# Optimization experiments

Measured on AMD Instinct MI355X. Metric: run time of the kernel, lower is better.

The kernel has to match this reference:

```python
import jax, jax.numpy as jnp
import numpy as np

N_NODES = 100000
N_EDGES = 1600000
IN_DIM, HID_DIM, OUT_DIM = 64, 128, 1


def gcn_conv(x, W, b, src, dst, n_nodes):
    """PyG-style GCNConv: h = x @ W; out = D^-1/2 (A+I) D^-1/2 h + b.
    Self-loops handled analytically (message h_i * dinv_i^2) to avoid
    concatenating them onto the edge list."""
    h = x @ W  # [N, F_out]
    ones = jnp.ones((src.shape[0],), dtype=x.dtype)
    deg = jax.ops.segment_sum(ones, dst, num_segments=n_nodes) + 1.0  # +1 self-loop
    dinv = jax.lax.rsqrt(deg)  # deg >= 1 so always finite
    norm = dinv[src] * dinv[dst]  # [E]
    msgs = h[src] * norm[:, None]  # [E, F_out] gather + scale
    agg = jax.ops.segment_sum(msgs, dst, num_segments=n_nodes)  # scatter-add
    agg = agg + h * (dinv * dinv)[:, None]  # self-loop contribution
    return agg + b


def setup_inputs() -> dict:
    key = jax.random.key(0)
    k1, k2, k3, k4 = jax.random.split(key, 4)
    x = jax.random.normal(k1, (N_NODES, IN_DIM), dtype=jnp.float32)
    edge_index = jax.random.randint(k2, (2, N_EDGES), 0, N_NODES, dtype=jnp.int64)
    # Glorot-ish init for weights
    W1 = jax.random.normal(k3, (IN_DIM, HID_DIM), dtype=jnp.float32) / np.sqrt(IN_DIM)
    b1 = jnp.zeros((HID_DIM,), dtype=jnp.float32)
    W2 = jax.random.normal(k4, (HID_DIM, OUT_DIM), dtype=jnp.float32) / np.sqrt(HID_DIM)
    b2 = jnp.zeros((OUT_DIM,), dtype=jnp.float32)
    return {"x": x, "edge_index": edge_index, "W1": W1, "b1": b1, "W2": W2, "b2": b2}


def reference(x, edge_index, W1, b1, W2, b2):
    src, dst = edge_index[0], edge_index[1]
    h = gcn_conv(x, W1, b1, src, dst, N_NODES)
    h = jax.nn.relu(h)
    # dropout(0.3) in eval mode == identity
    out = gcn_conv(h, W2, b2, src, dst, N_NODES)
    return out.reshape(-1)  # [N]
```

## Files before the change

### kernel.cpp

```cpp
#include <hip/hip_runtime.h>
#include <hip/hip_bf16.h>

#define NNODES 100000
#define NEDGES 1600000
#define IN_DIM 64
#define HID_DIM 128

#define BUKSHIFT 8
#define BUKNODES 256
#define NBUK ((NNODES + 255) >> 8)
#define BUKCAP 4608
#define CHUNK 4096
#define TILE_N 128
#define W1TS 72

#define EPACK(s, d)  ((s) | (((d) & 255) << 24))
#define ESRC(p)      ((p) & 0x00FFFFFF)
#define EDL(p)       ((int)(((unsigned)(p)) >> 24))

typedef __attribute__((ext_vector_type(8))) short short8;
typedef __attribute__((ext_vector_type(4))) float f32x4;

__device__ inline unsigned short f2bf(float f) {
    unsigned u = __float_as_uint(f);
    u += 0x7fff + ((u >> 16) & 1);
    return (unsigned short)(u >> 16);
}
__device__ inline unsigned bfpack2(float a, float b) {
    return (unsigned)f2bf(a) | ((unsigned)f2bf(b) << 16);
}
__device__ inline float bflo(unsigned u) { return __uint_as_float(u << 16); }
__device__ inline float bfhi(unsigned u) { return __uint_as_float(u & 0xffff0000u); }
__device__ inline float bfu16(unsigned v) { return __uint_as_float(v << 16); }

__global__ __launch_bounds__(1024, 8) void k_part(const int* __restrict__ src,
                                                  const int* __restrict__ dst,
                                                  int* __restrict__ gbcur,
                                                  int* __restrict__ ebuf, int E) {
    __shared__ int stage[CHUNK];
    __shared__ unsigned short bukof[CHUNK];
    __shared__ int hist[NBUK];
    __shared__ int scanb[NBUK];
    __shared__ int basep[NBUK];
    __shared__ int sb[2][512];
    int t = threadIdx.x;
    int start = blockIdx.x * CHUNK;
    int n = E - start; if (n > CHUNK) n = CHUNK;

    if (t < NBUK) hist[t] = 0;
    __syncthreads();

    int myb[4], myr[4], mp[4];
    #pragma unroll
    for (int i = 0; i < 4; i++) {
        int c = t + i * 1024;
        if (c < n) {
            int s = src[start + c];
            int d = dst[start + c];
            int b = d >> BUKSHIFT;
            myb[i] = b;
            mp[i]  = EPACK(s, d);
            myr[i] = atomicAdd(&hist[b], 1);
        } else myb[i] = -1;
    }
    __syncthreads();

    {
        int v = (t < NBUK) ? hist[t] : 0;
        if (t < 512) sb[0][t] = v;
        __syncthreads();
        int pin = 0;
        for (int ofs = 1; ofs < 512; ofs <<= 1) {
            if (t < 512) sb[pin ^ 1][t] = (t >= ofs) ? sb[pin][t] + sb[pin][t - ofs]
                                                     : sb[pin][t];
            __syncthreads();
            pin ^= 1;
        }
        if (t < NBUK) scanb[t] = sb[pin][t] - v;
    }

    if (t < NBUK) {
        int h = hist[t];
        basep[t] = h ? (t * BUKCAP + atomicAdd(&gbcur[t], h)) : 0;
    }
    __syncthreads();

    #pragma unroll
    for (int i = 0; i < 4; i++) {
        if (myb[i] >= 0) {
            int p = scanb[myb[i]] + myr[i];
            stage[p] = mp[i];
            bukof[p] = (unsigned short)myb[i];
        }
    }
    __syncthreads();

    for (int c = t; c < n; c += 1024) {
        int b = bukof[c];
        ebuf[basep[b] + (c - scanb[b])] = stage[c];
    }
}

__global__ __launch_bounds__(1024, 8) void k_bfill(const int* __restrict__ gbcur,
                                                   const int* __restrict__ ebuf,
                                                   const float* __restrict__ x,
                                                   int* __restrict__ off,
                                                   int* __restrict__ nend,
                                                   float* __restrict__ dinv,
                                                   int* __restrict__ csr,
                                                   unsigned* __restrict__ xsb, int N) {
    __shared__ int sEdge[BUKCAP];
    __shared__ int lcnt[BUKNODES];
    __shared__ int sbuf[2][BUKNODES];
    __shared__ int cur[BUKNODES];
    __shared__ float sdinv[BUKNODES];
    int b = blockIdx.x, t = threadIdx.x;
    int nbase = b << BUKSHIFT;
    int rbase = b * BUKCAP;
    int cntb = gbcur[b];
    if (t < BUKNODES) lcnt[t] = 0;
    __syncthreads();
    for (int i = t; i < cntb; i += 1024) {
        int p = ebuf[rbase + i];
        sEdge[i] = p;
        atomicAdd(&lcnt[EDL(p)], 1);
    }
    __syncthreads();
    int v = (t < BUKNODES) ? lcnt[t] : 0;
    if (t < BUKNODES) sbuf[0][t] = v;
    __syncthreads();
    int pin = 0;
    for (int ofs = 1; ofs < BUKNODES; ofs <<= 1) {
        if (t < BUKNODES) sbuf[pin ^ 1][t] = (t >= ofs) ? sbuf[pin][t] + sbuf[pin][t - ofs]
                                                        : sbuf[pin][t];
        __syncthreads();
        pin ^= 1;
    }
    if (t < BUKNODES) {
        int o = rbase + sbuf[pin][t] - v;
        int nid = nbase + t;
        float dv = rsqrtf((float)v + 1.0f);
        sdinv[t] = dv;
        if (nid < N) {
            off[nid]  = o;
            nend[nid] = o + v;
            dinv[nid] = dv;
        }
        cur[t] = o;
    }
    __syncthreads();
    for (int i = t; i < cntb; i += 1024) {
        int p = sEdge[i];
        int pos = atomicAdd(&cur[EDL(p)], 1);
        csr[pos] = ESRC(p);
    }
    for (int i = t; i < BUKNODES * 16; i += 1024) {
        int nl = i >> 4;
        int nid = nbase + nl;
        if (nid < N) {
            float dv = sdinv[nl];
            float4 vx = ((const float4*)x)[(size_t)nid * 16 + (i & 15)];
            uint2 u;
            u.x = bfpack2(vx.x * dv, vx.y * dv);
            u.y = bfpack2(vx.z * dv, vx.w * dv);
            ((uint2*)xsb)[(size_t)nid * 16 + (i & 15)] = u;
        }
    }
}

__global__ __launch_bounds__(256) void k_gathd(const int* __restrict__ off,
                                               const int* __restrict__ nend,
                                               const int* __restrict__ csr,
                                               const unsigned short* __restrict__ xsu,
                                               const float* __restrict__ dinv,
                                               unsigned short* __restrict__ aggu,
                                               int n_nodes) {
    int tid = blockIdx.x * 256 + threadIdx.x;
    int n = tid >> 6;
    if (n >= n_nodes) return;
    int lane = threadIdx.x & 63;
    int beg = off[n], fin = nend[n];
    float dd = dinv[n];

    float a0 = bfu16(xsu[(size_t)n * 64 + lane]);
    float a1 = 0.f, a2 = 0.f, a3 = 0.f;

    for (int base = beg; base < fin; base += 64) {
        int nn = fin - base; if (nn > 64) nn = 64;
        int idx = (lane < nn) ? csr[base + lane] : 0;
        int j = 0;
        for (; j + 4 <= nn; j += 4) {
            int s0 = __shfl(idx, j);
            int s1 = __shfl(idx, j + 1);
            int s2 = __shfl(idx, j + 2);
            int s3 = __shfl(idx, j + 3);
            unsigned v0 = xsu[(size_t)s0 * 64 + lane];
            unsigned v1 = xsu[(size_t)s1 * 64 + lane];
            unsigned v2 = xsu[(size_t)s2 * 64 + lane];
            unsigned v3 = xsu[(size_t)s3 * 64 + lane];
            a0 += bfu16(v0);
            a1 += bfu16(v1);
            a2 += bfu16(v2);
            a3 += bfu16(v3);
        }
        for (; j < nn; ++j) {
            int s = __shfl(idx, j);
            a0 += bfu16(xsu[(size_t)s * 64 + lane]);
        }
    }
    float r = ((a0 + a1) + (a2 + a3)) * dd;
    aggu[(size_t)n * 64 + lane] = f2bf(r);
}

__global__ __launch_bounds__(512) void k_mlp(const uint4* __restrict__ aggb,
                                             const float* __restrict__ W1,
                                             const float* __restrict__ b1,
                                             const float* __restrict__ W2,
                                             const float* __restrict__ dinv,
                                             float* __restrict__ zd, int n_nodes) {
    __shared__ __align__(16) unsigned short sW1t[HID_DIM * W1TS];
    __shared__ float sW2[HID_DIM];
    __shared__ float sb1[HID_DIM];
    int t = threadIdx.x;
    for (int i = t; i < IN_DIM * HID_DIM; i += 512) {
        int k = i >> 7, hid = i & 127;
        sW1t[hid * W1TS + k] = f2bf(W1[i]);
    }
    if (t < HID_DIM) { sW2[t] = W2[t]; sb1[t] = b1[t]; }
    __syncthreads();

    int node0 = blockIdx.x * TILE_N;
    int w = t >> 6;
    int lane = t & 63;
    int col = lane & 15;
    int quad = lane >> 4;

    int na = node0 + w * 16 + col;
    int nac = na < n_nodes ? na : 0;
    const short8* arow = (const short8*)(aggb + (size_t)nac * 8);
    short8 a0 = arow[quad];
    short8 a1 = arow[4 + quad];

    float zpart[4] = {0, 0, 0, 0};
    #pragma unroll
    for (int h0 = 0; h0 < 8; h0++) {
        int hid = h0 * 16 + col;
        const short8* brow = (const short8*)(sW1t + hid * W1TS);
        short8 b0 = brow[quad];
        short8 b1f = brow[4 + quad];
        f32x4 cc = {0.f, 0.f, 0.f, 0.f};
        cc = __builtin_amdgcn_mfma_f32_16x16x32_bf16(a0, b0, cc, 0, 0, 0);
        cc = __builtin_amdgcn_mfma_f32_16x16x32_bf16(a1, b1f, cc, 0, 0, 0);
        float bb = sb1[hid], ww = sW2[hid];
        #pragma unroll
        for (int r = 0; r < 4; r++) {
            float v = cc[r] + bb;
            zpart[r] += (v > 0.f ? v : 0.f) * ww;
        }
    }
    #pragma unroll
    for (int m = 1; m < 16; m <<= 1) {
        #pragma unroll
        for (int r = 0; r < 4; r++) zpart[r] += __shfl_xor(zpart[r], m);
    }
    if (col == 0) {
        #pragma unroll
        for (int r = 0; r < 4; r++) {
            int n = node0 + w * 16 + quad * 4 + r;
            if (n < n_nodes) zd[n] = zpart[r] * dinv[n];
        }
    }
}

__global__ __launch_bounds__(1024, 8) void k_gather1(const int* __restrict__ off,
                                                     const int* __restrict__ nend,
                                                     const int* __restrict__ csr,
                                                     const float* __restrict__ zd,
                                                     const float* __restrict__ dinv,
                                                     const float* __restrict__ b2,
                                                     float* __restrict__ out, int n_nodes) {
    int tid = blockIdx.x * 1024 + threadIdx.x;
    int n = tid >> 3;
    int l = tid & 7;
    if (n >= n_nodes) return;
    int beg = off[n], fin = nend[n];
    float a0 = 0.0f, a1 = 0.0f;
    for (int i = beg + l; i < fin; i += 16) {
        a0 += zd[csr[i]];
        int i2 = i + 8;
        if (i2 < fin) a1 += zd[csr[i2]];
    }
    float a = a0 + a1;
    a += __shfl_xor(a, 1);
    a += __shfl_xor(a, 2);
    a += __shfl_xor(a, 4);
    if (l == 0) out[n] = (a + zd[n]) * dinv[n] + b2[0];
}

extern "C" void kernel_launch(void* const* d_in, const int* in_sizes, int n_in,
                              void* d_out, int out_size, void* d_ws, size_t ws_size,
                              hipStream_t stream) {
    const float* x  = (const float*)d_in[0];
    const int*   ei = (const int*)d_in[1];
    const float* W1 = (const float*)d_in[2];
    const float* b1 = (const float*)d_in[3];
    const float* W2 = (const float*)d_in[4];
    const float* b2 = (const float*)d_in[5];
    float* out = (float*)d_out;

    const int N = NNODES;
    const int E = NEDGES;
    const int* src = ei;
    const int* dst = ei + E;

    int* gbcur = (int*)d_ws;
    int* off   = gbcur + 512;
    int* nend  = off + N;
    float* dinv = (float*)(nend + N);
    float* zd   = dinv + N;
    int* csr    = (int*)(zd + N);
    size_t o1 = ((size_t)((char*)(csr + NBUK * BUKCAP) - (char*)d_ws) + 127) & ~(size_t)127;
    unsigned* xsb = (unsigned*)((char*)d_ws + o1);
    size_t o2 = o1 + (size_t)N * 128;
    int*   ebuf = (int*)((char*)d_ws + o2);
    unsigned short* aggu = (unsigned short*)((char*)d_ws + o2);

    hipMemsetAsync(gbcur, 0, 512 * sizeof(int), stream);
    k_part<<<(E + CHUNK - 1) / CHUNK, 1024, 0, stream>>>(src, dst, gbcur, ebuf, E);
    k_bfill<<<NBUK, 1024, 0, stream>>>(gbcur, ebuf, x, off, nend, dinv, csr, xsb, N);
    k_gathd<<<(N * 64 + 255) / 256, 256, 0, stream>>>(off, nend, csr,
                                                      (const unsigned short*)xsb, dinv,
                                                      aggu, N);
    k_mlp<<<(N + TILE_N - 1) / TILE_N, 512, 0, stream>>>((const uint4*)aggu, W1, b1, W2,
                                                         dinv, zd, N);
    k_gather1<<<(N * 8 + 1023) / 1024, 1024, 0, stream>>>(off, nend, csr, zd, dinv, b2, out, N);
}
```

Before: 177.9 us.

## Replace CSR gather with bucketed LDS integer-atomic aggregation on int16-quantized features

The first-layer aggregation no longer does a per-node CSR gather. It now runs one block per 128-node bucket, reading the bucketed edge buffer directly and accumulating neighbour features into shared memory with integer atomics. The pre-scaled features are stored as fixed-point int16 (scale 4096, clamped) instead of bf16, which makes the integer LDS atomics exact and order-independent. Bucket size is halved to keep the accumulator in LDS, and the partition scan is widened to match. The risks are LDS atomic contention, precision loss and clamping for large scaled inputs, and a bucket capacity of 2432 that may overflow for skewed degree distributions.

```diff
diff --git a/kernel.cpp b/kernel.cpp
--- a/kernel.cpp
+++ b/kernel.cpp
@@ -6,15 +6,17 @@
 #define IN_DIM 64
 #define HID_DIM 128
 
-#define BUKSHIFT 8
-#define BUKNODES 256
-#define NBUK ((NNODES + 255) >> 8)
-#define BUKCAP 4608
+#define BUKSHIFT 7
+#define BUKNODES 128
+#define NBUK ((NNODES + 127) >> 7)
+#define BUKCAP 2432
 #define CHUNK 4096
 #define TILE_N 128
 #define W1TS 72
-
-#define EPACK(s, d)  ((s) | (((d) & 255) << 24))
+#define ACCS 66
+#define QS 4096.0f
+
+#define EPACK(s, d)  ((s) | (((d) & 127) << 24))
 #define ESRC(p)      ((p) & 0x00FFFFFF)
 #define EDL(p)       ((int)(((unsigned)(p)) >> 24))
 
@@ -29,9 +31,10 @@
 __device__ inline unsigned bfpack2(float a, float b) {
     return (unsigned)f2bf(a) | ((unsigned)f2bf(b) << 16);
 }
-__device__ inline float bflo(unsigned u) { return __uint_as_float(u << 16); }
-__device__ inline float bfhi(unsigned u) { return __uint_as_float(u & 0xffff0000u); }
-__device__ inline float bfu16(unsigned v) { return __uint_as_float(v << 16); }
+__device__ inline int f2i12(float v) {
+    float c = fminf(fmaxf(v * QS, -32767.f), 32767.f);
+    return __float2int_rn(c);
+}
 
 __global__ __launch_bounds__(1024, 8) void k_part(const int* __restrict__ src,
                                                   const int* __restrict__ dst,
@@ -42,7 +45,7 @@
     __shared__ int hist[NBUK];
     __shared__ int scanb[NBUK];
     __shared__ int basep[NBUK];
-    __shared__ int sb[2][512];
+    __shared__ int sb[2][1024];
     int t = threadIdx.x;
     int start = blockIdx.x * CHUNK;
     int n = E - start; if (n > CHUNK) n = CHUNK;
@@ -67,12 +70,11 @@
 
     {
         int v = (t < NBUK) ? hist[t] : 0;
-        if (t < 512) sb[0][t] = v;
+        sb[0][t] = v;
         __syncthreads();
         int pin = 0;
-        for (int ofs = 1; ofs < 512; ofs <<= 1) {
-            if (t < 512) sb[pin ^ 1][t] = (t >= ofs) ? sb[pin][t] + sb[pin][t - ofs]
-                                                     : sb[pin][t];
+        for (int ofs = 1; ofs < 1024; ofs <<= 1) {
+            sb[pin ^ 1][t] = (t >= ofs) ? sb[pin][t] + sb[pin][t - ofs] : sb[pin][t];
             __syncthreads();
             pin ^= 1;
         }
@@ -108,7 +110,7 @@
                                                    int* __restrict__ nend,
                                                    float* __restrict__ dinv,
                                                    int* __restrict__ csr,
-                                                   unsigned* __restrict__ xsb, int N) {
+                                                   short* __restrict__ xsq, int N) {
     __shared__ int sEdge[BUKCAP];
     __shared__ int lcnt[BUKNODES];
     __shared__ int sbuf[2][BUKNODES];
@@ -160,56 +162,77 @@
         if (nid < N) {
             float dv = sdinv[nl];
             float4 vx = ((const float4*)x)[(size_t)nid * 16 + (i & 15)];
+            int q0 = f2i12(vx.x * dv), q1 = f2i12(vx.y * dv);
+            int q2 = f2i12(vx.z * dv), q3 = f2i12(vx.w * dv);
             uint2 u;
-            u.x = bfpack2(vx.x * dv, vx.y * dv);
-            u.y = bfpack2(vx.z * dv, vx.w * dv);
-            ((uint2*)xsb)[(size_t)nid * 16 + (i & 15)] = u;
-        }
-    }
-}
-
-__global__ __launch_bounds__(256) void k_gathd(const int* __restrict__ off,
-                                               const int* __restrict__ nend,
-                                               const int* __restrict__ csr,
-                                               const unsigned short* __restrict__ xsu,
-                                               const float* __restrict__ dinv,
-                                               unsigned short* __restrict__ aggu,
-                                               int n_nodes) {
-    int tid = blockIdx.x * 256 + threadIdx.x;
-    int n = tid >> 6;
-    if (n >= n_nodes) return;
-    int lane = threadIdx.x & 63;
-    int beg = off[n], fin = nend[n];
-    float dd = dinv[n];
-
-    float a0 = bfu16(xsu[(size_t)n * 64 + lane]);
-    float a1 = 0.f, a2 = 0.f, a3 = 0.f;
-
-    for (int base = beg; base < fin; base += 64) {
-        int nn = fin - base; if (nn > 64) nn = 64;
-        int idx = (lane < nn) ? csr[base + lane] : 0;
-        int j = 0;
-        for (; j + 4 <= nn; j += 4) {
-            int s0 = __shfl(idx, j);
-            int s1 = __shfl(idx, j + 1);
-            int s2 = __shfl(idx, j + 2);
-            int s3 = __shfl(idx, j + 3);
-            unsigned v0 = xsu[(size_t)s0 * 64 + lane];
-            unsigned v1 = xsu[(size_t)s1 * 64 + lane];
-            unsigned v2 = xsu[(size_t)s2 * 64 + lane];
-            unsigned v3 = xsu[(size_t)s3 * 64 + lane];
-            a0 += bfu16(v0);
-            a1 += bfu16(v1);
-            a2 += bfu16(v2);
-            a3 += bfu16(v3);
-        }
-        for (; j < nn; ++j) {
-            int s = __shfl(idx, j);
-            a0 += bfu16(xsu[(size_t)s * 64 + lane]);
-        }
-    }
-    float r = ((a0 + a1) + (a2 + a3)) * dd;
-    aggu[(size_t)n * 64 + lane] = f2bf(r);
+            u.x = (q0 & 0xffff) | (q1 << 16);
+            u.y = (q2 & 0xffff) | (q3 << 16);
+            ((uint2*)xsq)[(size_t)nid * 16 + (i & 15)] = u;
+        }
+    }
+}
+
+__global__ __launch_bounds__(512, 8) void k_agg(const int* __restrict__ gbcur,
+                                                const int* __restrict__ ebuf,
+                                                const short* __restrict__ xsq,
+                                                const float* __restrict__ dinv,
+                                                unsigned short* __restrict__ aggu, int N) {
+    __shared__ int acc[BUKNODES * ACCS];
+    int b = blockIdx.x, t = threadIdx.x;
+    int rbase = b * BUKCAP;
+    int cntb = gbcur[b];
+    for (int i = t; i < BUKNODES * ACCS; i += 512) acc[i] = 0;
+    __syncthreads();
+
+    int c = t & 7;
+    int g = t >> 3;
+    const uint4* xq4 = (const uint4*)xsq;
+    for (int base = 0; base < cntb; base += 128) {
+        int e0 = base + g, e1 = base + 64 + g;
+        bool v0 = e0 < cntb, v1 = e1 < cntb;
+        int p0 = v0 ? ebuf[rbase + e0] : 0;
+        int p1 = v1 ? ebuf[rbase + e1] : 0;
+        uint4 ua = {0, 0, 0, 0}, ub = {0, 0, 0, 0};
+        if (v0) ua = xq4[(size_t)ESRC(p0) * 8 + c];
+        if (v1) ub = xq4[(size_t)ESRC(p1) * 8 + c];
+        if (v0) {
+            int* ar = &acc[EDL(p0) * ACCS + c * 8];
+            atomicAdd(&ar[0], (int)(short)(ua.x & 0xffff));
+            atomicAdd(&ar[1], ((int)ua.x) >> 16);
+            atomicAdd(&ar[2], (int)(short)(ua.y & 0xffff));
+            atomicAdd(&ar[3], ((int)ua.y) >> 16);
+            atomicAdd(&ar[4], (int)(short)(ua.z & 0xffff));
+            atomicAdd(&ar[5], ((int)ua.z) >> 16);
+            atomicAdd(&ar[6], (int)(short)(ua.w & 0xffff));
+            atomicAdd(&ar[7], ((int)ua.w) >> 16);
+        }
+        if (v1) {
+            int* ar = &acc[EDL(p1) * ACCS + c * 8];
+            atomicAdd(&ar[0], (int)(short)(ub.x & 0xffff));
+            atomicAdd(&ar[1], ((int)ub.x) >> 16);
+            atomicAdd(&ar[2], (int)(short)(ub.y & 0xffff));
+            atomicAdd(&ar[3], ((int)ub.y) >> 16);
+            atomicAdd(&ar[4], (int)(short)(ub.z & 0xffff));
+            atomicAdd(&ar[5], ((int)ub.z) >> 16);
+            atomicAdd(&ar[6], (int)(short)(ub.w & 0xffff));
+            atomicAdd(&ar[7], ((int)ub.w) >> 16);
+        }
+    }
+    __syncthreads();
+
+    int nbase = b << BUKSHIFT;
+    for (int i = t; i < BUKNODES * 32; i += 512) {
+        int dl = i >> 5, dp = i & 31;
+        int n = nbase + dl;
+        if (n < N) {
+            float dd = dinv[n] * (1.0f / QS);
+            int sp = ((const int*)xsq)[(size_t)n * 32 + dp];
+            int s0 = (sp << 16) >> 16, s1 = sp >> 16;
+            int A0 = acc[dl * ACCS + 2 * dp], A1 = acc[dl * ACCS + 2 * dp + 1];
+            ((unsigned*)aggu)[(size_t)n * 32 + dp] =
+                bfpack2((float)(A0 + s0) * dd, (float)(A1 + s1) * dd);
+        }
+    }
 }
 
 __global__ __launch_bounds__(512) void k_mlp(const uint4* __restrict__ aggb,
@@ -314,23 +337,22 @@
     const int* dst = ei + E;
 
     int* gbcur = (int*)d_ws;
-    int* off   = gbcur + 512;
+    int* off   = gbcur + 1024;
     int* nend  = off + N;
     float* dinv = (float*)(nend + N);
     float* zd   = dinv + N;
     int* csr    = (int*)(zd + N);
     size_t o1 = ((size_t)((char*)(csr + NBUK * BUKCAP) - (char*)d_ws) + 127) & ~(size_t)127;
-    unsigned* xsb = (unsigned*)((char*)d_ws + o1);
+    short* xsq = (short*)((char*)d_ws + o1);
     size_t o2 = o1 + (size_t)N * 128;
-    int*   ebuf = (int*)((char*)d_ws + o2);
-    unsigned short* aggu = (unsigned short*)((char*)d_ws + o2);
-
-    hipMemsetAsync(gbcur, 0, 512 * sizeof(int), stream);
+    int* ebuf  = (int*)((char*)d_ws + o2);
+    size_t o3 = ((o2 + (size_t)NBUK * BUKCAP * 4) + 127) & ~(size_t)127;
+    unsigned short* aggu = (unsigned short*)((char*)d_ws + o3);
+
+    hipMemsetAsync(gbcur, 0, 1024 * sizeof(int), stream);
     k_part<<<(E + CHUNK - 1) / CHUNK, 1024, 0, stream>>>(src, dst, gbcur, ebuf, E);
-    k_bfill<<<NBUK, 1024, 0, stream>>>(gbcur, ebuf, x, off, nend, dinv, csr, xsb, N);
-    k_gathd<<<(N * 64 + 255) / 256, 256, 0, stream>>>(off, nend, csr,
-                                                      (const unsigned short*)xsb, dinv,
-                                                      aggu, N);
+    k_bfill<<<NBUK, 1024, 0, stream>>>(gbcur, ebuf, x, off, nend, dinv, csr, xsq, N);
+    k_agg<<<NBUK, 512, 0, stream>>>(gbcur, ebuf, xsq, dinv, aggu, N);
     k_mlp<<<(N + TILE_N - 1) / TILE_N, 512, 0, stream>>>((const uint4*)aggu, W1, b1, W2,
                                                          dinv, zd, N);
     k_gather1<<<(N * 8 + 1023) / 1024, 1024, 0, stream>>>(off, nend, csr, zd, dinv, b2, out, N);
```

New measurement: 175.8 us. About the same (-1.2%).
